# Optimization experiments

Hardware: AMD Instinct MI355X
Metric: run time of the kernel (lower is better)

## Reference

```python
import jax, jax.numpy as jnp
import numpy as np

F_NUM, F_DIM, O_DIM, K = 16, 32, 2, 16
B, T, C = 256, 48, 3000
V = K + 2  # code vocabulary: 0 unused, 1 = missing, 2..K+1 = centroid ids
NEG_BIG = 1e7


def setup_inputs() -> dict:
    key = jax.random.key(0)
    ks = jax.random.split(key, 16)
    return {
        "tdata": jax.random.normal(ks[0], (B, T, F_NUM, F_DIM), jnp.float32),
        "f_mask": jax.random.randint(ks[1], (B, T, F_NUM), 0, 2) > 0,
        "centers": jax.random.normal(ks[2], (F_NUM, K, F_DIM), jnp.float32),
        "pat": jax.random.randint(ks[3], (F_NUM, C, F_NUM), 0, V),
        "pat_rep": jax.random.normal(ks[4], (F_NUM, C, F_DIM), jnp.float32),
        "pos_cnt": jax.random.uniform(ks[5], (F_NUM, C), jnp.float32),
        "neg_cnt": jax.random.uniform(ks[6], (F_NUM, C), jnp.float32),
        "W_q": jax.random.normal(ks[7], (F_NUM, F_DIM, F_DIM), jnp.float32) * 0.1,
        "b_q": jax.random.normal(ks[8], (F_NUM, F_DIM), jnp.float32) * 0.1,
        "W_k": jax.random.normal(ks[9], (F_NUM, F_DIM, F_DIM + 1), jnp.float32) * 0.1,
        "b_k": jax.random.normal(ks[10], (F_NUM, F_DIM), jnp.float32) * 0.1,
        "W_v": jax.random.normal(ks[11], (F_NUM, F_DIM + 1, F_DIM + 1), jnp.float32) * 0.1,
        "b_v": jax.random.normal(ks[12], (F_NUM, F_DIM + 1), jnp.float32) * 0.1,
        "W_pred": jax.random.normal(ks[13], (O_DIM, F_NUM * (F_DIM + 1)), jnp.float32) * 0.1,
    }


def _forward(tdata, f_mask, centers, pat, pat_rep, pos_cnt, neg_cnt,
             W_q, b_q, W_k, b_k, W_v, b_v, W_pred):
    Bs, Ts, Fn, D = tdata.shape
    N = Bs * Ts
    fdata = tdata.reshape(N, Fn, D)

    # --- compute_codes: nearest-centroid assignment per feature (vectorized) ---
    # dist[n,i,k] = ||fdata[n,i]||^2 - 2 <fdata[n,i], centers[i,k]> + ||centers[i,k]||^2
    d_norm = jnp.sum(fdata * fdata, axis=-1, keepdims=True)            # [N,F,1]
    c_norm = jnp.sum(centers * centers, axis=-1)                        # [F,K]
    dots = jnp.einsum('nid,ikd->nik', fdata, centers)                   # [N,F,K]
    dists = d_norm - 2.0 * dots + c_norm[None]                          # [N,F,K]
    pos_codes = jnp.argmin(dists, axis=-1) + 2                          # [N,F]
    maskNF = f_mask.reshape(N, Fn)
    f_codes = jnp.where(maskNF, pos_codes, 1)                           # [N,F] int, 1 = missing

    # one-hot codes, shared across feature loop: [N, F, V]
    oh = jax.nn.one_hot(f_codes, V, dtype=jnp.float32)

    q_last = tdata[:, -1]                                               # [B,F,D]
    reps, atts = [], []
    for i in range(Fn):
        pat_i = pat[i]                                                  # [C,F]
        # A[c,j,v]=1 iff pattern slot is wildcard (0) or code v matches pat
        eq = jnp.arange(V)[None, None, :] == pat_i[:, :, None]
        A = jnp.where((pat_i == 0)[:, :, None], True, eq).astype(jnp.float32)
        # count of matching slots; match iff all F slots match
        cnt = jnp.einsum('njv,cjv->nc', oh, A)                          # [N,C]
        match_nc = cnt >= (Fn - 0.5)
        pm = jnp.any(match_nc.reshape(Bs, Ts, C), axis=1)               # [B,C] any over time
        pm_f = pm.astype(jnp.float32)

        pos_ratio = pos_cnt[i] / (pos_cnt[i] + neg_cnt[i] + 1e-6)       # [C]
        rep_aug = jnp.concatenate([pat_rep[i], pos_ratio[:, None]], 1)  # [C,D+1]
        key_i = pm_f[:, :, None] * rep_aug[None]                        # [B,C,D+1]

        # FinalAttentionQKV, attention_type='mul'
        iq = q_last[:, i] @ W_q[i].T + b_q[i]                           # [B,D]
        ik = key_i @ W_k[i].T + b_k[i]                                  # [B,C,D]
        iv = key_i @ W_v[i].T + b_v[i]                                  # [B,C,D+1]
        e = jnp.einsum('bcd,bd->bc', ik, iq)
        e = e - (1.0 - pm_f) * NEG_BIG
        a = jax.nn.softmax(e, axis=-1)
        v = jnp.einsum('bc,bce->be', a, iv)                             # [B,D+1]
        reps.append(v)
        atts.append(a)

    rep = jnp.stack(reps, axis=1)                                       # [B,F,D+1]
    rep = rep * jnp.any(f_mask, axis=1)[:, :, None].astype(rep.dtype)
    cohort_cali = rep.reshape(Bs, -1) @ W_pred.T                        # [B,o_dim]
    cohort_a = jnp.stack(atts, axis=0)                                  # [F,B,C]
    return cohort_cali, cohort_a, rep


def reference(tdata, f_mask, centers, pat, pat_rep, pos_cnt, neg_cnt,
              W_q, b_q, W_k, b_k, W_v, b_v, W_pred):
    return _forward(tdata, f_mask, centers, pat, pat_rep, pos_cnt, neg_cnt,
                    W_q, b_q, W_k, b_k, W_v, b_v, W_pred)
```

## Files before the change

### kernel.cpp

```cpp
#include <hip/hip_runtime.h>
#include <stdint.h>

#define FN 16
#define FD 32
#define KC 16
#define BS 256
#define TS 48
#define CS 3000
#define VV 18
#define NW 96
#define NEG_BIG 10000000.0f

__global__ __launch_bounds__(64) void k_codes(const float* __restrict__ tdata,
                                              const int* __restrict__ f_mask,
                                              const float* __restrict__ centers,
                                              uint8_t* __restrict__ codes) {
    __shared__ float xs[64][33];
    __shared__ float cns[KC];
    int t   = threadIdx.x;
    int bid = blockIdx.x;
    int j   = bid & 15;
    int n0  = (bid >> 4) << 6;

    const float* cen = centers + (size_t)j * KC * FD;

    if (t < KC) {
        float cn = 0.f;
#pragma unroll
        for (int d = 0; d < FD; d++) { float cv = cen[t * FD + d]; cn += cv * cv; }
        cns[t] = cn;
    }
#pragma unroll
    for (int it = 0; it < 8; ++it) {
        int f = t + (it << 6);
        int row = f >> 3, q = f & 7;
        float4 v = *reinterpret_cast<const float4*>(
            tdata + ((size_t)(n0 + row) * FN + j) * FD + (q << 2));
        xs[row][(q << 2) + 0] = v.x;
        xs[row][(q << 2) + 1] = v.y;
        xs[row][(q << 2) + 2] = v.z;
        xs[row][(q << 2) + 3] = v.w;
    }
    __syncthreads();

    float xv[FD];
#pragma unroll
    for (int d = 0; d < FD; d++) xv[d] = xs[t][d];

    float best = 3.4e38f; int bestk = 0;
    for (int k = 0; k < KC; k++) {
        float dot = 0.f;
#pragma unroll
        for (int d = 0; d < FD; d++) dot += xv[d] * cen[k * FD + d];
        float dist = cns[k] - 2.f * dot;
        if (dist < best) { best = dist; bestk = k; }
    }
    int idx = (n0 + t) * FN + j;
    codes[idx] = f_mask[idx] ? (uint8_t)(bestk + 2) : (uint8_t)1;
}

__global__ __launch_bounds__(64) void k_buildM(const int* __restrict__ pat,
                                               uint32_t* __restrict__ M) {
    int lane = threadIdx.x;
    int bid  = blockIdx.x;
    int i = bid / 47, g = bid % 47;
    int c = (g << 6) + lane;
    bool valid = (c < CS);
    for (int j = 0; j < FN; j++) {
        int p = valid ? pat[((size_t)i * CS + c) * FN + j] : -1;
        bool wild = (p == 0);
        uint32_t* dst = M + (((size_t)((i << 4) | j) * VV) * NW) + (g << 1);
        for (int v = 0; v < VV; v++) {
            unsigned long long bal = __ballot(wild || (p == v));
            if (lane < 2) dst[(size_t)v * NW + lane] =
                (lane == 0) ? (uint32_t)bal : (uint32_t)(bal >> 32);
        }
    }
}

__global__ __launch_bounds__(96) void k_match(const uint8_t* __restrict__ codes,
                                              const uint32_t* __restrict__ M,
                                              uint32_t* __restrict__ pm) {
    int b = blockIdx.x & 255;
    int i = blockIdx.x >> 8;
    int cg = threadIdx.x;
    __shared__ uint8_t cs[TS * FN];
    __shared__ uint32_t mrow[VV * NW];

    for (int k = cg; k < TS * FN; k += 96)
        cs[k] = codes[(size_t)b * TS * FN + k];

    uint32_t m[TS];
#pragma unroll
    for (int t = 0; t < TS; t++) m[t] = 0xFFFFFFFFu;

    const uint32_t* Mi = M + (size_t)i * FN * VV * NW;
    for (int j = 0; j < FN; j++) {
        __syncthreads();
        const uint32_t* src = Mi + (size_t)j * VV * NW;
#pragma unroll
        for (int r = 0; r < VV; r++) mrow[r * NW + cg] = src[r * NW + cg];
        __syncthreads();

        uint32_t any = 0;
#pragma unroll
        for (int t = 0; t < TS; t++) {
            int v = cs[t * FN + j];
            m[t] &= mrow[v * NW + cg];
            any |= m[t];
        }
        if (!__syncthreads_or(any != 0u)) break;
    }

    uint32_t acc = 0;
#pragma unroll
    for (int t = 0; t < TS; t++) acc |= m[t];
    pm[(size_t)blockIdx.x * NW + cg] = acc;
}

__global__ __launch_bounds__(256) void k_attn(
    const float* __restrict__ tdata, const float* __restrict__ pat_rep,
    const float* __restrict__ pos_cnt, const float* __restrict__ neg_cnt,
    const float* __restrict__ W_q, const float* __restrict__ b_q,
    const float* __restrict__ W_k, const float* __restrict__ b_k,
    const float* __restrict__ W_v, const float* __restrict__ b_v,
    const uint32_t* __restrict__ pm, const int* __restrict__ f_mask,
    float* __restrict__ out_a, float* __restrict__ out_rep)
{
    int b = blockIdx.x & 255;
    int i = blockIdx.x >> 8;
    int tid = threadIdx.x;

    __shared__ float e_s[CS];
    __shared__ float iq_s[FD];
    __shared__ float kq_s[FD + 1];
    __shared__ float s_sh[FD + 1];
    __shared__ float red[4];
    __shared__ float bkiq_s, maxv_s, sum_s;
    __shared__ int any_s;

    int mbit = (tid < TS) ? f_mask[((size_t)b * TS + tid) * FN + i] : 0;
    unsigned long long bal = __ballot(mbit != 0);
    if (tid == 0) any_s = (bal != 0ULL);

    const float* q = tdata + (((size_t)b * TS + (TS - 1)) * FN + i) * FD;
    if (tid >= 64 && tid < 64 + FD) {
        int r = tid - 64;
        float acc = b_q[i * FD + r];
        const float* Wr = W_q + ((size_t)i * FD + r) * FD;
#pragma unroll
        for (int e = 0; e < FD; e++) acc += q[e] * Wr[e];
        iq_s[r] = acc;
    }
    if (tid < FD + 1) s_sh[tid] = 0.f;
    __syncthreads();
    if (tid < FD + 1) {
        float acc = 0.f;
        for (int d = 0; d < FD; d++)
            acc += W_k[((size_t)i * FD + d) * (FD + 1) + tid] * iq_s[d];
        kq_s[tid] = acc;
    }
    if (tid == 64) {
        float acc = 0.f;
        for (int d = 0; d < FD; d++) acc += b_k[i * FD + d] * iq_s[d];
        bkiq_s = acc;
    }
    __syncthreads();
    float bkiq = bkiq_s;

    const uint32_t* pmrow = pm + (size_t)blockIdx.x * NW;

    float lmax = -3.4e38f;
    for (int c = tid; c < CS; c += 256) {
        uint32_t bit = (pmrow[c >> 5] >> (c & 31)) & 1u;
        float e;
        if (bit) {
            const float* pr = pat_rep + ((size_t)i * CS + c) * FD;
            float acc = 0.f;
#pragma unroll
            for (int d = 0; d < FD; d++) acc += pr[d] * kq_s[d];
            float pc = pos_cnt[(size_t)i * CS + c], nc = neg_cnt[(size_t)i * CS + c];
            float ratio = pc / (pc + nc + 1e-6f);
            e = bkiq + acc + ratio * kq_s[FD];
        } else {
            e = bkiq - NEG_BIG;
        }
        e_s[c] = e;
        lmax = fmaxf(lmax, e);
    }
    for (int off = 32; off > 0; off >>= 1) lmax = fmaxf(lmax, __shfl_down(lmax, off));
    if ((tid & 63) == 0) red[tid >> 6] = lmax;
    __syncthreads();
    if (tid == 0) {
        float m = red[0];
        for (int w = 1; w < 4; w++) m = fmaxf(m, red[w]);
        maxv_s = m;
    }
    __syncthreads();
    float maxv = maxv_s;

    float lsum = 0.f;
    for (int c = tid; c < CS; c += 256) {
        float ex = __expf(e_s[c] - maxv);
        e_s[c] = ex;
        lsum += ex;
    }
    for (int off = 32; off > 0; off >>= 1) lsum += __shfl_down(lsum, off);
    if ((tid & 63) == 0) red[tid >> 6] = lsum;
    __syncthreads();
    if (tid == 0) sum_s = red[0] + red[1] + red[2] + red[3];
    __syncthreads();
    float sum = sum_s;

    float* arow = out_a + (size_t)blockIdx.x * CS;
    for (int c = tid; c < CS; c += 256) {
        float a = e_s[c] / sum;
        arow[c] = a;
        uint32_t bit = (pmrow[c >> 5] >> (c & 31)) & 1u;
        if (bit) {
            const float* pr = pat_rep + ((size_t)i * CS + c) * FD;
            for (int f = 0; f < FD; f++) atomicAdd(&s_sh[f], a * pr[f]);
            float pc = pos_cnt[(size_t)i * CS + c], nc = neg_cnt[(size_t)i * CS + c];
            float ratio = pc / (pc + nc + 1e-6f);
            atomicAdd(&s_sh[FD], a * ratio);
        }
    }
    __syncthreads();

    if (tid < FD + 1) {
        float acc = b_v[(size_t)i * (FD + 1) + tid];
        const float* Wr = W_v + ((size_t)i * (FD + 1) + tid) * (FD + 1);
#pragma unroll
        for (int f = 0; f < FD + 1; f++) acc += Wr[f] * s_sh[f];
        float r = any_s ? acc : 0.f;
        out_rep[((size_t)b * FN + i) * (FD + 1) + tid] = r;
    }
}

__global__ __launch_bounds__(256) void k_cali(const float* __restrict__ rep,
                                              const float* __restrict__ W_pred,
                                              float* __restrict__ out) {
    int b = blockIdx.x;
    int tid = threadIdx.x;
    const int KK = FN * (FD + 1);
    float a0 = 0.f, a1 = 0.f;
    for (int k = tid; k < KK; k += 256) {
        float r = rep[(size_t)b * KK + k];
        a0 += r * W_pred[k];
        a1 += r * W_pred[KK + k];
    }
    for (int off = 32; off > 0; off >>= 1) {
        a0 += __shfl_down(a0, off);
        a1 += __shfl_down(a1, off);
    }
    __shared__ float r0[4], r1[4];
    if ((tid & 63) == 0) { r0[tid >> 6] = a0; r1[tid >> 6] = a1; }
    __syncthreads();
    if (tid == 0) {
        out[b * 2 + 0] = r0[0] + r0[1] + r0[2] + r0[3];
        out[b * 2 + 1] = r1[0] + r1[1] + r1[2] + r1[3];
    }
}

extern "C" void kernel_launch(void* const* d_in, const int* in_sizes, int n_in,
                              void* d_out, int out_size, void* d_ws, size_t ws_size,
                              hipStream_t stream) {
    const float* tdata   = (const float*)d_in[0];
    const int*   f_mask  = (const int*)d_in[1];
    const float* centers = (const float*)d_in[2];
    const int*   pat     = (const int*)d_in[3];
    const float* pat_rep = (const float*)d_in[4];
    const float* pos_cnt = (const float*)d_in[5];
    const float* neg_cnt = (const float*)d_in[6];
    const float* W_q     = (const float*)d_in[7];
    const float* b_q     = (const float*)d_in[8];
    const float* W_k     = (const float*)d_in[9];
    const float* b_k     = (const float*)d_in[10];
    const float* W_v     = (const float*)d_in[11];
    const float* b_v     = (const float*)d_in[12];
    const float* W_pred  = (const float*)d_in[13];

    float* out = (float*)d_out;
    float* out_cali = out;
    float* out_a    = out + 512;
    float* out_rep  = out + 512 + FN * BS * CS;

    char* ws = (char*)d_ws;
    uint8_t*  codes = (uint8_t*)ws;
    uint32_t* M     = (uint32_t*)(ws + 200704);
    uint32_t* pm    = (uint32_t*)(ws + 200704 + 1769472);

    hipLaunchKernelGGL(k_codes,   dim3(16 * 192), dim3(64), 0, stream,
                       tdata, f_mask, centers, codes);
    hipLaunchKernelGGL(k_buildM,  dim3(16 * 47), dim3(64), 0, stream,
                       pat, M);
    hipLaunchKernelGGL(k_match,   dim3(FN * BS), dim3(NW), 0, stream,
                       codes, M, pm);
    hipLaunchKernelGGL(k_attn,    dim3(FN * BS), dim3(256), 0, stream,
                       tdata, pat_rep, pos_cnt, neg_cnt, W_q, b_q, W_k, b_k, W_v, b_v,
                       pm, f_mask, out_a, out_rep);
    hipLaunchKernelGGL(k_cali,    dim3(BS), dim3(256), 0, stream,
                       out_rep, W_pred, out_cali);
}
```

Baseline: 244.7 us.

## Rebuild pattern bitmasks via LDS transpose and match directly from global memory

After: 214.7 us. 12.3% less time.

```diff
diff --git a/kernel.cpp b/kernel.cpp
--- a/kernel.cpp
+++ b/kernel.cpp
@@ -59,63 +59,79 @@
     codes[idx] = f_mask[idx] ? (uint8_t)(bestk + 2) : (uint8_t)1;
 }
 
-__global__ __launch_bounds__(64) void k_buildM(const int* __restrict__ pat,
-                                               uint32_t* __restrict__ M) {
-    int lane = threadIdx.x;
-    int bid  = blockIdx.x;
-    int i = bid / 47, g = bid % 47;
-    int c = (g << 6) + lane;
-    bool valid = (c < CS);
-    for (int j = 0; j < FN; j++) {
-        int p = valid ? pat[((size_t)i * CS + c) * FN + j] : -1;
-        bool wild = (p == 0);
-        uint32_t* dst = M + (((size_t)((i << 4) | j) * VV) * NW) + (g << 1);
-        for (int v = 0; v < VV; v++) {
-            unsigned long long bal = __ballot(wild || (p == v));
-            if (lane < 2) dst[(size_t)v * NW + lane] =
-                (lane == 0) ? (uint32_t)bal : (uint32_t)(bal >> 32);
-        }
-    }
-}
-
-__global__ __launch_bounds__(96) void k_match(const uint8_t* __restrict__ codes,
-                                              const uint32_t* __restrict__ M,
-                                              uint32_t* __restrict__ pm) {
+__global__ __launch_bounds__(128) void k_buildM(const int* __restrict__ pat,
+                                                uint32_t* __restrict__ M) {
+    __shared__ int pl[256 * 17];
+    int tid = threadIdx.x;
+    int i  = blockIdx.x / 12;
+    int ch = blockIdx.x % 12;
+    int c0 = ch << 8;
+
+    for (int f = tid; f < 256 * 16; f += 128) {
+        int r = f >> 4, jj = f & 15;
+        int c = c0 + r;
+        pl[r * 17 + jj] = (c < CS) ? pat[((size_t)i * CS + c) * FN + jj] : -1;
+    }
+    __syncthreads();
+
+    int w = tid >> 4, j = tid & 15;
+    int p[32];
+#pragma unroll
+    for (int cb = 0; cb < 32; cb++) p[cb] = pl[((w << 5) + cb) * 17 + j];
+
+    uint32_t w0 = 0u;
+#pragma unroll
+    for (int cb = 0; cb < 32; cb++) w0 |= (p[cb] == 0) ? (1u << cb) : 0u;
+
+    uint32_t* dst = M + ((size_t)((i << 4) | j) * VV) * NW + (ch << 3) + w;
+#pragma unroll
+    for (int v = 0; v < VV; v++) {
+        uint32_t wv = w0;
+#pragma unroll
+        for (int cb = 0; cb < 32; cb++) wv |= (p[cb] == v) ? (1u << cb) : 0u;
+        dst[(size_t)v * NW] = wv;
+    }
+}
+
+__global__ __launch_bounds__(128) void k_match(const uint8_t* __restrict__ codes,
+                                               const uint32_t* __restrict__ M,
+                                               uint32_t* __restrict__ pm) {
     int b = blockIdx.x & 255;
     int i = blockIdx.x >> 8;
-    int cg = threadIdx.x;
-    __shared__ uint8_t cs[TS * FN];
-    __shared__ uint32_t mrow[VV * NW];
-
-    for (int k = cg; k < TS * FN; k += 96)
-        cs[k] = codes[(size_t)b * TS * FN + k];
+    int tid = threadIdx.x;
+    __shared__ uint16_t cs16[FN][TS];
+
+    for (int f = tid; f < TS * FN; f += 128) {
+        int t = f >> 4, jj = f & 15;
+        cs16[jj][t] = (uint16_t)codes[(size_t)b * TS * FN + f] * (uint16_t)(NW * 4);
+    }
+    __syncthreads();
 
     uint32_t m[TS];
 #pragma unroll
     for (int t = 0; t < TS; t++) m[t] = 0xFFFFFFFFu;
 
-    const uint32_t* Mi = M + (size_t)i * FN * VV * NW;
+    int lane = tid & 63;
+    const char* Mi = (const char*)(M + (size_t)i * FN * VV * NW);
+    size_t cgb = (size_t)tid << 2;
+
     for (int j = 0; j < FN; j++) {
-        __syncthreads();
-        const uint32_t* src = Mi + (size_t)j * VV * NW;
-#pragma unroll
-        for (int r = 0; r < VV; r++) mrow[r * NW + cg] = src[r * NW + cg];
-        __syncthreads();
-
+        int vv = (lane < TS) ? (int)cs16[j][lane] : 0;
+        const char* page = Mi + (size_t)j * (VV * NW * 4);
         uint32_t any = 0;
 #pragma unroll
         for (int t = 0; t < TS; t++) {
-            int v = cs[t * FN + j];
-            m[t] &= mrow[v * NW + cg];
+            int sv = __builtin_amdgcn_readlane(vv, t);
+            m[t] &= *(const uint32_t*)(page + sv + cgb);
             any |= m[t];
         }
-        if (!__syncthreads_or(any != 0u)) break;
+        if (__ballot(any != 0u) == 0ULL) break;
     }
 
     uint32_t acc = 0;
 #pragma unroll
     for (int t = 0; t < TS; t++) acc |= m[t];
-    pm[(size_t)blockIdx.x * NW + cg] = acc;
+    if (tid < NW) pm[(size_t)blockIdx.x * NW + tid] = acc;
 }
 
 __global__ __launch_bounds__(256) void k_attn(
@@ -292,9 +308,9 @@
 
     hipLaunchKernelGGL(k_codes,   dim3(16 * 192), dim3(64), 0, stream,
                        tdata, f_mask, centers, codes);
-    hipLaunchKernelGGL(k_buildM,  dim3(16 * 47), dim3(64), 0, stream,
+    hipLaunchKernelGGL(k_buildM,  dim3(16 * 12), dim3(128), 0, stream,
                        pat, M);
-    hipLaunchKernelGGL(k_match,   dim3(FN * BS), dim3(NW), 0, stream,
+    hipLaunchKernelGGL(k_match,   dim3(FN * BS), dim3(128), 0, stream,
                        codes, M, pm);
     hipLaunchKernelGGL(k_attn,    dim3(FN * BS), dim3(256), 0, stream,
                        tdata, pat_rep, pos_cnt, neg_cnt, W_q, b_q, W_k, b_k, W_v, b_v,
```
